# Kernel tuning notes

Hardware: AMD Instinct MI355X
Metric: run time of the kernel (lower is better)

Reference implementation:

```python
import jax, jax.numpy as jnp
import numpy as np
import math

N_CLASSES = 1000
CODE_LENGTH = 1024
IN_FEATURES = 4096
BATCH = 512
MAX_PROB = 0.95
POWER = 1.0


def _hadamard(n):
    # Sylvester construction; n must be a power of 2.
    H = np.array([[1.0]], dtype=np.float64)
    while H.shape[0] < n:
        H = np.block([[H, H], [H, -H]])
    return H


def setup_inputs() -> dict:
    key = jax.random.key(0)
    k1, k2, k3 = jax.random.split(key, 3)
    x = jax.random.normal(k1, (BATCH, IN_FEATURES), dtype=jnp.float32)
    out_feat = CODE_LENGTH - 1  # single head: code_length//1 - 1
    # nn.Linear default init: U(-1/sqrt(fan_in), 1/sqrt(fan_in))
    bound = 1.0 / math.sqrt(IN_FEATURES)
    W = jax.random.uniform(k2, (out_feat, IN_FEATURES), dtype=jnp.float32, minval=-bound, maxval=bound)
    b = jax.random.uniform(k3, (out_feat,), dtype=jnp.float32, minval=-bound, maxval=bound)
    labels = jnp.asarray(_hadamard(CODE_LENGTH)[:N_CLASSES, 1:], dtype=jnp.float32)  # (C, L-1)
    eps = jnp.float32(CODE_LENGTH * math.pow((1.0 - MAX_PROB) / (MAX_PROB * (N_CLASSES - 1)), 1.0 / POWER))
    power = jnp.float32(POWER)
    return {"x": x, "W": W, "b": b, "labels": labels, "eps": eps, "power": power}


def reference(x, W, b, labels, eps, power):
    # Linear head: (B, in) @ (in, L-1) + b
    h = jnp.tanh(x @ W.T + b)                               # (B, L-1)
    # L1 distance to each Hadamard code row: (B, 1, L-1) vs (C, L-1)
    d = jnp.sum(jnp.abs(h[:, None, :] - labels), axis=-1)   # (B, C)
    d = jnp.maximum(d, eps)
    inv = 1.0 / jnp.power(d, power)                          # (B, C)
    return inv / jnp.sum(inv, axis=-1, keepdims=True)
```

## Files before the change

### kernel.cpp

```cpp
#include <hip/hip_runtime.h>

#define BATCH 512
#define INFEAT 4096
#define LOUT 1023
#define NCLS 1000
#define NPAD 1024
#define SPLITK 8

typedef __bf16 bf16x8 __attribute__((ext_vector_type(8)));
typedef float f32x4 __attribute__((ext_vector_type(4)));

__device__ __forceinline__ unsigned short f2bf(float a) {
    unsigned u = __builtin_bit_cast(unsigned, a);
    return (unsigned short)((u + 0x7fffu + ((u >> 16) & 1u)) >> 16);
}
__device__ __forceinline__ unsigned f2bf2(float a, float b) {
    return (unsigned)f2bf(a) | ((unsigned)f2bf(b) << 16);
}
__device__ __forceinline__ float bf2f(unsigned short u) {
    return __builtin_bit_cast(float, ((unsigned)u) << 16);
}

__device__ __forceinline__ void gload_lds16(const void* g, void* l) {
    __builtin_amdgcn_global_load_lds(
        (const __attribute__((address_space(1))) void*)g,
        (__attribute__((address_space(3))) void*)l, 16, 0, 0);
}

__global__ __launch_bounds__(256) void k_cvt(const float* __restrict__ x,
                                             const float* __restrict__ W,
                                             unsigned char* __restrict__ xb,
                                             unsigned char* __restrict__ Wb) {
    int blk = blockIdx.x;
    if (blk < 1024) {
        int g = blk * 256 + threadIdx.x;
        int r = g >> 9, k16 = g & 511;
        const float4* p = (const float4*)(x + (size_t)r * INFEAT + k16 * 8);
        float4 v0 = p[0], v1 = p[1];
        uint4 o;
        o.x = f2bf2(v0.x, v0.y); o.y = f2bf2(v0.z, v0.w);
        o.z = f2bf2(v1.x, v1.y); o.w = f2bf2(v1.z, v1.w);
        *(uint4*)(xb + (size_t)r * 8192 + (k16 >> 3) * 128 + (((k16 & 7) ^ (r & 7)) * 16)) = o;
    } else {
        int g = (blk - 1024) * 256 + threadIdx.x;
        int r = g >> 9, k16 = g & 511;
        uint4 o = {0, 0, 0, 0};
        if (r < LOUT) {
            const float4* p = (const float4*)(W + (size_t)r * INFEAT + k16 * 8);
            float4 v0 = p[0], v1 = p[1];
            o.x = f2bf2(v0.x, v0.y); o.y = f2bf2(v0.z, v0.w);
            o.z = f2bf2(v1.x, v1.y); o.w = f2bf2(v1.z, v1.w);
        }
        *(uint4*)(Wb + (size_t)r * 8192 + (k16 >> 3) * 128 + (((k16 & 7) ^ (r & 7)) * 16)) = o;
    }
}

__global__ __launch_bounds__(256, 2) void k_gemm1(
    const unsigned char* __restrict__ xb, const unsigned char* __restrict__ Wb,
    unsigned short* __restrict__ partial) {
    __shared__ unsigned char lds[49152];
    f32x4 acc[4][2] = {};
    const int bn = blockIdx.x, bm = blockIdx.y, sp = blockIdx.z;
    const int tid = threadIdx.x;
    const int wave = tid >> 6, lane = tid & 63;
    const int lrow = lane & 15, lgrp = lane >> 4;
    const int wr = wave >> 1, wc = wave & 1;
    const int arow0 = bm * 128, brow0 = bn * 64, chunk0 = sp * 8;

    auto STAGE = [&](int bsel, int c) {
        unsigned char* lA = lds + bsel * 24576;
        unsigned char* lB = lA + 16384;
#pragma unroll
        for (int rr = 0; rr < 4; ++rr) {
            int g = rr * 256 + tid;
            int r = g >> 3, s = g & 7;
            gload_lds16(xb + (size_t)(arow0 + r) * 8192 + c * 128 + s * 16,
                        lA + (rr * 256 + wave * 64) * 16);
        }
#pragma unroll
        for (int rr = 0; rr < 2; ++rr) {
            int g = rr * 256 + tid;
            int r = g >> 3, s = g & 7;
            gload_lds16(Wb + (size_t)(brow0 + r) * 8192 + c * 128 + s * 16,
                        lB + (rr * 256 + wave * 64) * 16);
        }
    };

    auto COMPUTE = [&](int bsel) {
        const unsigned char* lA = lds + bsel * 24576;
        const unsigned char* lB = lA + 16384;
#pragma unroll
        for (int ks = 0; ks < 2; ++ks) {
            int swz = ((ks * 4 + lgrp) ^ (lrow & 7)) * 16;
            bf16x8 a[4], b[2];
#pragma unroll
            for (int m = 0; m < 4; ++m)
                a[m] = *(const bf16x8*)(lA + (wr * 64 + m * 16 + lrow) * 128 + swz);
#pragma unroll
            for (int n = 0; n < 2; ++n)
                b[n] = *(const bf16x8*)(lB + (wc * 32 + n * 16 + lrow) * 128 + swz);
#pragma unroll
            for (int m = 0; m < 4; ++m)
#pragma unroll
                for (int n = 0; n < 2; ++n)
                    acc[m][n] = __builtin_amdgcn_mfma_f32_16x16x32_bf16(
                        a[m], b[n], acc[m][n], 0, 0, 0);
        }
    };

    STAGE(0, chunk0);
    asm volatile("s_waitcnt vmcnt(0)" ::: "memory");
    __syncthreads();
#pragma unroll 1
    for (int t = 0; t < 8; ++t) {
        int cur = t & 1;
        if (t + 1 < 8) STAGE(cur ^ 1, chunk0 + t + 1);
        COMPUTE(cur);
        asm volatile("s_waitcnt vmcnt(0)" ::: "memory");
        __syncthreads();
    }

    unsigned short* P = partial + (size_t)sp * (BATCH * NPAD);
#pragma unroll
    for (int m = 0; m < 4; ++m)
#pragma unroll
        for (int n = 0; n < 2; ++n)
#pragma unroll
            for (int reg = 0; reg < 4; ++reg) {
                int r = arow0 + wr * 64 + m * 16 + lgrp * 4 + reg;
                int c = brow0 + wc * 32 + n * 16 + lrow;
                P[(size_t)r * NPAD + c] = f2bf(acc[m][n][reg]);
            }
}

__global__ __launch_bounds__(256) void k_fused(const unsigned short* __restrict__ partial,
                                               const float* __restrict__ bias,
                                               const float* __restrict__ epsp,
                                               const float* __restrict__ powp,
                                               float* __restrict__ out) {
    __shared__ float g[1024];
    __shared__ float wsum[4];
    const int r = blockIdx.x, t = threadIdx.x;
    const int n0 = t * 4;

    f32x4 v = {0.0f, 0.0f, 0.0f, 0.0f};
#pragma unroll
    for (int s = 0; s < SPLITK; ++s) {
        ushort4 p = *(const ushort4*)(partial + ((size_t)s * BATCH + r) * NPAD + n0);
        v[0] += bf2f(p.x); v[1] += bf2f(p.y); v[2] += bf2f(p.z); v[3] += bf2f(p.w);
    }
    float bb[4];
    if (t < 255) {
        float4 b4 = *(const float4*)(bias + n0);
        bb[0] = b4.x; bb[1] = b4.y; bb[2] = b4.z; bb[3] = b4.w;
    } else {
        bb[0] = bias[1020]; bb[1] = bias[1021]; bb[2] = bias[1022]; bb[3] = 0.0f;
    }
    if (t == 0) g[0] = 0.0f;
#pragma unroll
    for (int j = 0; j < 4; ++j) {
        int n = n0 + j;
        if (n < LOUT) g[n + 1] = tanhf(v[j] + bb[j]);
    }
    __syncthreads();

#pragma unroll 1
    for (int s = 0; s < 10; ++s) {
        int st = 1 << s;
#pragma unroll
        for (int pp = 0; pp < 2; ++pp) {
            int p = t + pp * 256;
            int idx = ((p >> s) << (s + 1)) | (p & (st - 1));
            float a = g[idx], c = g[idx + st];
            g[idx] = a + c;
            g[idx + st] = a - c;
        }
        __syncthreads();
    }

    const float eps = *epsp, pw = *powp;
    float iv[4];
    float ss = 0.0f;
#pragma unroll
    for (int j = 0; j < 4; ++j) {
        int c = n0 + j;
        float d = fmaxf(1023.0f - g[c], eps);
        float q = (pw == 1.0f) ? (1.0f / d) : powf(d, -pw);
        if (c >= NCLS) q = 0.0f;
        iv[j] = q;
        ss += q;
    }
#pragma unroll
    for (int m = 32; m; m >>= 1) ss += __shfl_xor(ss, m, 64);
    if ((t & 63) == 0) wsum[t >> 6] = ss;
    __syncthreads();
    float sc = 1.0f / (wsum[0] + wsum[1] + wsum[2] + wsum[3]);

    if (n0 < NCLS) {
        float4 o;
        o.x = iv[0] * sc; o.y = iv[1] * sc; o.z = iv[2] * sc; o.w = iv[3] * sc;
        *(float4*)(out + (size_t)r * NCLS + n0) = o;
    }
}

extern "C" void kernel_launch(void* const* d_in, const int* in_sizes, int n_in,
                              void* d_out, int out_size, void* d_ws, size_t ws_size,
                              hipStream_t stream) {
    const float* x = (const float*)d_in[0];
    const float* W = (const float*)d_in[1];
    const float* b = (const float*)d_in[2];
    const float* epsp = (const float*)d_in[4];
    const float* powp = (const float*)d_in[5];
    float* out = (float*)d_out;

    unsigned char* ws = (unsigned char*)d_ws;
    unsigned char* xb = ws;
    unsigned char* Wb = ws + (4u << 20);
    unsigned short* partial = (unsigned short*)(ws + (12u << 20));

    k_cvt<<<3072, 256, 0, stream>>>(x, W, xb, Wb);
    k_gemm1<<<dim3(16, 4, 8), 256, 0, stream>>>(xb, Wb, partial);
    k_fused<<<512, 256, 0, stream>>>(partial, b, epsp, powp, out);
}
```

Measured before the change: 27.93 us.

## Fuse split-K GEMM and epilogue via grid barrier, triple-buffer K stages

Merges the split-K GEMM and the tanh/Hadamard/normalize epilogue into one persistent 512-block kernel. A global atomic counter, reset by the conversion kernel, acts as a grid-wide barrier, so one launch is saved. The GEMM pipeline moves from double to triple buffering with partial vmcnt waits and raw barriers, keeping two loads in flight. Block indices are remapped so split-K slices interleave across CUs. This relies on all 512 blocks being co-resident: with 77.8KB LDS per block it could deadlock if occupancy is lower than assumed.

```diff
diff --git a/kernel.cpp b/kernel.cpp
--- a/kernel.cpp
+++ b/kernel.cpp
@@ -6,6 +6,7 @@
 #define NCLS 1000
 #define NPAD 1024
 #define SPLITK 8
+#define NBLK 512
 
 typedef __bf16 bf16x8 __attribute__((ext_vector_type(8)));
 typedef float f32x4 __attribute__((ext_vector_type(4)));
@@ -30,8 +31,10 @@
 __global__ __launch_bounds__(256) void k_cvt(const float* __restrict__ x,
                                              const float* __restrict__ W,
                                              unsigned char* __restrict__ xb,
-                                             unsigned char* __restrict__ Wb) {
+                                             unsigned char* __restrict__ Wb,
+                                             int* __restrict__ done) {
     int blk = blockIdx.x;
+    if (blk == 0 && threadIdx.x == 0) *done = 0;
     if (blk < 1024) {
         int g = blk * 256 + threadIdx.x;
         int r = g >> 9, k16 = g & 511;
@@ -55,32 +58,41 @@
     }
 }
 
-__global__ __launch_bounds__(256, 2) void k_gemm1(
+__global__ __launch_bounds__(256, 2) void k_gemm_fused(
     const unsigned char* __restrict__ xb, const unsigned char* __restrict__ Wb,
-    unsigned short* __restrict__ partial) {
-    __shared__ unsigned char lds[49152];
-    f32x4 acc[4][2] = {};
-    const int bn = blockIdx.x, bm = blockIdx.y, sp = blockIdx.z;
+    unsigned short* __restrict__ partial, const float* __restrict__ bias,
+    const float* __restrict__ epsp, const float* __restrict__ powp,
+    float* __restrict__ out, int* __restrict__ done) {
+    extern __shared__ __align__(16) unsigned char smem[];
+    unsigned char* lds = smem;
+    float* g = (float*)(smem + 73728);
+    float* wsum = (float*)(smem + 77824);
+
+    const int bid = blockIdx.x;
+    const int work = (bid & 7) * 64 + (bid >> 3);
+    const int bn = work & 15, bm = (work >> 4) & 3, sp = work >> 6;
     const int tid = threadIdx.x;
     const int wave = tid >> 6, lane = tid & 63;
     const int lrow = lane & 15, lgrp = lane >> 4;
     const int wr = wave >> 1, wc = wave & 1;
     const int arow0 = bm * 128, brow0 = bn * 64, chunk0 = sp * 8;
 
+    f32x4 acc[4][2] = {};
+
     auto STAGE = [&](int bsel, int c) {
         unsigned char* lA = lds + bsel * 24576;
         unsigned char* lB = lA + 16384;
 #pragma unroll
         for (int rr = 0; rr < 4; ++rr) {
-            int g = rr * 256 + tid;
-            int r = g >> 3, s = g & 7;
+            int gg = rr * 256 + tid;
+            int r = gg >> 3, s = gg & 7;
             gload_lds16(xb + (size_t)(arow0 + r) * 8192 + c * 128 + s * 16,
                         lA + (rr * 256 + wave * 64) * 16);
         }
 #pragma unroll
         for (int rr = 0; rr < 2; ++rr) {
-            int g = rr * 256 + tid;
-            int r = g >> 3, s = g & 7;
+            int gg = rr * 256 + tid;
+            int r = gg >> 3, s = gg & 7;
             gload_lds16(Wb + (size_t)(brow0 + r) * 8192 + c * 128 + s * 16,
                         lB + (rr * 256 + wave * 64) * 16);
         }
@@ -109,15 +121,23 @@
     };
 
     STAGE(0, chunk0);
-    asm volatile("s_waitcnt vmcnt(0)" ::: "memory");
-    __syncthreads();
+    STAGE(1, chunk0 + 1);
 #pragma unroll 1
     for (int t = 0; t < 8; ++t) {
-        int cur = t & 1;
-        if (t + 1 < 8) STAGE(cur ^ 1, chunk0 + t + 1);
-        COMPUTE(cur);
-        asm volatile("s_waitcnt vmcnt(0)" ::: "memory");
-        __syncthreads();
+        if (t < 6) {
+            STAGE((t + 2) % 3, chunk0 + t + 2);
+            asm volatile("s_waitcnt vmcnt(12)" ::: "memory");
+        } else if (t == 6) {
+            asm volatile("s_waitcnt vmcnt(6)" ::: "memory");
+        } else {
+            asm volatile("s_waitcnt vmcnt(0)" ::: "memory");
+        }
+        __builtin_amdgcn_s_barrier();
+        asm volatile("" ::: "memory");
+        COMPUTE(t % 3);
+        asm volatile("s_waitcnt lgkmcnt(0)" ::: "memory");
+        __builtin_amdgcn_s_barrier();
+        asm volatile("" ::: "memory");
     }
 
     unsigned short* P = partial + (size_t)sp * (BATCH * NPAD);
@@ -131,17 +151,20 @@
                 int c = brow0 + wc * 32 + n * 16 + lrow;
                 P[(size_t)r * NPAD + c] = f2bf(acc[m][n][reg]);
             }
-}
-
-__global__ __launch_bounds__(256) void k_fused(const unsigned short* __restrict__ partial,
-                                               const float* __restrict__ bias,
-                                               const float* __restrict__ epsp,
-                                               const float* __restrict__ powp,
-                                               float* __restrict__ out) {
-    __shared__ float g[1024];
-    __shared__ float wsum[4];
-    const int r = blockIdx.x, t = threadIdx.x;
-    const int n0 = t * 4;
+
+    __syncthreads();
+    if (tid == 0) {
+        __threadfence();
+        atomicAdd(done, 1);
+        while (__hip_atomic_load(done, __ATOMIC_RELAXED,
+                                 __HIP_MEMORY_SCOPE_AGENT) < NBLK)
+            __builtin_amdgcn_s_sleep(1);
+        __threadfence();
+    }
+    __syncthreads();
+
+    const int r = work;
+    const int n0 = tid * 4;
 
     f32x4 v = {0.0f, 0.0f, 0.0f, 0.0f};
 #pragma unroll
@@ -150,13 +173,13 @@
         v[0] += bf2f(p.x); v[1] += bf2f(p.y); v[2] += bf2f(p.z); v[3] += bf2f(p.w);
     }
     float bb[4];
-    if (t < 255) {
+    if (tid < 255) {
         float4 b4 = *(const float4*)(bias + n0);
         bb[0] = b4.x; bb[1] = b4.y; bb[2] = b4.z; bb[3] = b4.w;
     } else {
         bb[0] = bias[1020]; bb[1] = bias[1021]; bb[2] = bias[1022]; bb[3] = 0.0f;
     }
-    if (t == 0) g[0] = 0.0f;
+    if (tid == 0) g[0] = 0.0f;
 #pragma unroll
     for (int j = 0; j < 4; ++j) {
         int n = n0 + j;
@@ -169,7 +192,7 @@
         int st = 1 << s;
 #pragma unroll
         for (int pp = 0; pp < 2; ++pp) {
-            int p = t + pp * 256;
+            int p = tid + pp * 256;
             int idx = ((p >> s) << (s + 1)) | (p & (st - 1));
             float a = g[idx], c = g[idx + st];
             g[idx] = a + c;
@@ -192,7 +215,7 @@
     }
 #pragma unroll
     for (int m = 32; m; m >>= 1) ss += __shfl_xor(ss, m, 64);
-    if ((t & 63) == 0) wsum[t >> 6] = ss;
+    if ((tid & 63) == 0) wsum[tid >> 6] = ss;
     __syncthreads();
     float sc = 1.0f / (wsum[0] + wsum[1] + wsum[2] + wsum[3]);
 
@@ -217,8 +240,9 @@
     unsigned char* xb = ws;
     unsigned char* Wb = ws + (4u << 20);
     unsigned short* partial = (unsigned short*)(ws + (12u << 20));
-
-    k_cvt<<<3072, 256, 0, stream>>>(x, W, xb, Wb);
-    k_gemm1<<<dim3(16, 4, 8), 256, 0, stream>>>(xb, Wb, partial);
-    k_fused<<<512, 256, 0, stream>>>(partial, b, epsp, powp, out);
-}
+    int* done = (int*)(ws + (20u << 20));
+
+    k_cvt<<<3072, 256, 0, stream>>>(x, W, xb, Wb, done);
+    k_gemm_fused<<<NBLK, 256, 77840, stream>>>(xb, Wb, partial, b, epsp, powp,
+                                               out, done);
+}
```

Measured after the change: 62.95 us. 2.25x slower.

## Fuse fp32-to-bf16 conversion into GEMM loads via register staging

Applied to the files above, without the earlier changes.

Removes the separate conversion kernel. The GEMM now reads fp32 x and W directly into registers, packs them to bf16 and writes them into swizzled LDS, with the next chunk's global loads overlapping the current MFMA compute. It also remaps the block index so split-K slices are interleaved across the grid. This saves one launch and the bf16 workspace round trip. In exchange, each block reads twice the global bytes, uses more registers, and loses the asynchronous direct-to-LDS loads.

```diff
diff --git a/kernel.cpp b/kernel.cpp
--- a/kernel.cpp
+++ b/kernel.cpp
@@ -14,75 +14,77 @@
     unsigned u = __builtin_bit_cast(unsigned, a);
     return (unsigned short)((u + 0x7fffu + ((u >> 16) & 1u)) >> 16);
 }
-__device__ __forceinline__ unsigned f2bf2(float a, float b) {
-    return (unsigned)f2bf(a) | ((unsigned)f2bf(b) << 16);
-}
 __device__ __forceinline__ float bf2f(unsigned short u) {
     return __builtin_bit_cast(float, ((unsigned)u) << 16);
 }
 
-__device__ __forceinline__ void gload_lds16(const void* g, void* l) {
-    __builtin_amdgcn_global_load_lds(
-        (const __attribute__((address_space(1))) void*)g,
-        (__attribute__((address_space(3))) void*)l, 16, 0, 0);
-}
-
-__global__ __launch_bounds__(256) void k_cvt(const float* __restrict__ x,
-                                             const float* __restrict__ W,
-                                             unsigned char* __restrict__ xb,
-                                             unsigned char* __restrict__ Wb) {
-    int blk = blockIdx.x;
-    if (blk < 1024) {
-        int g = blk * 256 + threadIdx.x;
-        int r = g >> 9, k16 = g & 511;
-        const float4* p = (const float4*)(x + (size_t)r * INFEAT + k16 * 8);
-        float4 v0 = p[0], v1 = p[1];
-        uint4 o;
-        o.x = f2bf2(v0.x, v0.y); o.y = f2bf2(v0.z, v0.w);
-        o.z = f2bf2(v1.x, v1.y); o.w = f2bf2(v1.z, v1.w);
-        *(uint4*)(xb + (size_t)r * 8192 + (k16 >> 3) * 128 + (((k16 & 7) ^ (r & 7)) * 16)) = o;
-    } else {
-        int g = (blk - 1024) * 256 + threadIdx.x;
-        int r = g >> 9, k16 = g & 511;
-        uint4 o = {0, 0, 0, 0};
-        if (r < LOUT) {
-            const float4* p = (const float4*)(W + (size_t)r * INFEAT + k16 * 8);
-            float4 v0 = p[0], v1 = p[1];
-            o.x = f2bf2(v0.x, v0.y); o.y = f2bf2(v0.z, v0.w);
-            o.z = f2bf2(v1.x, v1.y); o.w = f2bf2(v1.z, v1.w);
-        }
-        *(uint4*)(Wb + (size_t)r * 8192 + (k16 >> 3) * 128 + (((k16 & 7) ^ (r & 7)) * 16)) = o;
-    }
-}
-
-__global__ __launch_bounds__(256, 2) void k_gemm1(
-    const unsigned char* __restrict__ xb, const unsigned char* __restrict__ Wb,
+__device__ __forceinline__ uint4 pack8(float4 a, float4 b) {
+    union { __bf16 h[8]; uint4 u; } r;
+    r.h[0] = (__bf16)a.x; r.h[1] = (__bf16)a.y;
+    r.h[2] = (__bf16)a.z; r.h[3] = (__bf16)a.w;
+    r.h[4] = (__bf16)b.x; r.h[5] = (__bf16)b.y;
+    r.h[6] = (__bf16)b.z; r.h[7] = (__bf16)b.w;
+    return r.u;
+}
+
+__global__ __launch_bounds__(256, 2) void k_gemm(
+    const float* __restrict__ x, const float* __restrict__ W,
     unsigned short* __restrict__ partial) {
     __shared__ unsigned char lds[49152];
-    f32x4 acc[4][2] = {};
-    const int bn = blockIdx.x, bm = blockIdx.y, sp = blockIdx.z;
+    const int bid = blockIdx.x;
+    const int work = (bid & 7) * 64 + (bid >> 3);
+    const int bn = work & 15, bm = (work >> 4) & 3, sp = work >> 6;
     const int tid = threadIdx.x;
     const int wave = tid >> 6, lane = tid & 63;
     const int lrow = lane & 15, lgrp = lane >> 4;
     const int wr = wave >> 1, wc = wave & 1;
     const int arow0 = bm * 128, brow0 = bn * 64, chunk0 = sp * 8;
 
-    auto STAGE = [&](int bsel, int c) {
+    f32x4 acc[4][2] = {};
+    float4 ar[4][2], br[2][2];
+
+    auto LOADR = [&](int t) {
+        const int c = chunk0 + t;
+#pragma unroll
+        for (int rr = 0; rr < 4; ++rr) {
+            int g = rr * 256 + tid;
+            int row = g >> 3, j = g & 7;
+            const float4* p = (const float4*)(x + (size_t)(arow0 + row) * INFEAT
+                                              + c * 64 + j * 8);
+            ar[rr][0] = p[0]; ar[rr][1] = p[1];
+        }
+#pragma unroll
+        for (int rr = 0; rr < 2; ++rr) {
+            int g = rr * 256 + tid;
+            int row = g >> 3, j = g & 7;
+            int wrow = brow0 + row;
+            if (wrow < LOUT) {
+                const float4* p = (const float4*)(W + (size_t)wrow * INFEAT
+                                                  + c * 64 + j * 8);
+                br[rr][0] = p[0]; br[rr][1] = p[1];
+            } else {
+                br[rr][0] = make_float4(0.f, 0.f, 0.f, 0.f);
+                br[rr][1] = make_float4(0.f, 0.f, 0.f, 0.f);
+            }
+        }
+    };
+
+    auto WRITE = [&](int bsel) {
         unsigned char* lA = lds + bsel * 24576;
         unsigned char* lB = lA + 16384;
 #pragma unroll
         for (int rr = 0; rr < 4; ++rr) {
             int g = rr * 256 + tid;
-            int r = g >> 3, s = g & 7;
-            gload_lds16(xb + (size_t)(arow0 + r) * 8192 + c * 128 + s * 16,
-                        lA + (rr * 256 + wave * 64) * 16);
+            int row = g >> 3, j = g & 7;
+            *(uint4*)(lA + row * 128 + ((j ^ (row & 7)) * 16)) =
+                pack8(ar[rr][0], ar[rr][1]);
         }
 #pragma unroll
         for (int rr = 0; rr < 2; ++rr) {
             int g = rr * 256 + tid;
-            int r = g >> 3, s = g & 7;
-            gload_lds16(Wb + (size_t)(brow0 + r) * 8192 + c * 128 + s * 16,
-                        lB + (rr * 256 + wave * 64) * 16);
+            int row = g >> 3, j = g & 7;
+            *(uint4*)(lB + row * 128 + ((j ^ (row & 7)) * 16)) =
+                pack8(br[rr][0], br[rr][1]);
         }
     };
 
@@ -108,15 +110,14 @@
         }
     };
 
-    STAGE(0, chunk0);
-    asm volatile("s_waitcnt vmcnt(0)" ::: "memory");
+    LOADR(0);
+    WRITE(0);
     __syncthreads();
 #pragma unroll 1
     for (int t = 0; t < 8; ++t) {
-        int cur = t & 1;
-        if (t + 1 < 8) STAGE(cur ^ 1, chunk0 + t + 1);
-        COMPUTE(cur);
-        asm volatile("s_waitcnt vmcnt(0)" ::: "memory");
+        if (t + 1 < 8) LOADR(t + 1);
+        COMPUTE(t & 1);
+        if (t + 1 < 8) WRITE((t + 1) & 1);
         __syncthreads();
     }
 
@@ -214,11 +215,8 @@
     float* out = (float*)d_out;
 
     unsigned char* ws = (unsigned char*)d_ws;
-    unsigned char* xb = ws;
-    unsigned char* Wb = ws + (4u << 20);
-    unsigned short* partial = (unsigned short*)(ws + (12u << 20));
-
-    k_cvt<<<3072, 256, 0, stream>>>(x, W, xb, Wb);
-    k_gemm1<<<dim3(16, 4, 8), 256, 0, stream>>>(xb, Wb, partial);
+    unsigned short* partial = (unsigned short*)ws;
+
+    k_gemm<<<512, 256, 0, stream>>>(x, W, partial);
     k_fused<<<512, 256, 0, stream>>>(partial, b, epsp, powp, out);
 }
```

Measured after the change: 26.83 us. -3.9%, faster.

## Shrink GEMM tile to 64x64, raise occupancy, remap block indices

Applied to the files above, without the earlier changes.

The split-K GEMM tile shrinks from 128x64 to 64x64, which doubles the grid to 1024 blocks. The shared-memory buffer and accumulators are reduced so more blocks fit per CU (launch bounds raised to 5). Blocks are remapped with an interleaved 1D index so that consecutive blocks are spread across split-K slices, and LDS fragment loads are hoisted ahead of the MFMA chain with setprio. The aim is better CU utilisation and latency hiding on a small GEMM, at the cost of more redundant global/LDS loads per FLOP.

```diff
diff --git a/kernel.cpp b/kernel.cpp
--- a/kernel.cpp
+++ b/kernel.cpp
@@ -55,79 +55,85 @@
     }
 }
 
-__global__ __launch_bounds__(256, 2) void k_gemm1(
+__global__ __launch_bounds__(256, 5) void k_gemm(
     const unsigned char* __restrict__ xb, const unsigned char* __restrict__ Wb,
     unsigned short* __restrict__ partial) {
-    __shared__ unsigned char lds[49152];
-    f32x4 acc[4][2] = {};
-    const int bn = blockIdx.x, bm = blockIdx.y, sp = blockIdx.z;
+    __shared__ unsigned char lds[32768];
+    const int bid = blockIdx.x;
+    const int work = (bid & 7) * 128 + (bid >> 3);
+    const int bn = work & 15, bm = (work >> 4) & 7, sp = work >> 7;
     const int tid = threadIdx.x;
     const int wave = tid >> 6, lane = tid & 63;
     const int lrow = lane & 15, lgrp = lane >> 4;
     const int wr = wave >> 1, wc = wave & 1;
-    const int arow0 = bm * 128, brow0 = bn * 64, chunk0 = sp * 8;
+    const int arow0 = bm * 64, brow0 = bn * 64, chunk0 = sp * 8;
+
+    const int g0 = wave * 2 * 64 + lane;
+    const int g1 = (wave * 2 + 1) * 64 + lane;
+    const int r0 = g0 >> 3, s0 = g0 & 7;
+    const int r1 = g1 >> 3, s1 = g1 & 7;
+
+    f32x4 acc[2][2] = {};
 
     auto STAGE = [&](int bsel, int c) {
-        unsigned char* lA = lds + bsel * 24576;
-        unsigned char* lB = lA + 16384;
-#pragma unroll
-        for (int rr = 0; rr < 4; ++rr) {
-            int g = rr * 256 + tid;
-            int r = g >> 3, s = g & 7;
-            gload_lds16(xb + (size_t)(arow0 + r) * 8192 + c * 128 + s * 16,
-                        lA + (rr * 256 + wave * 64) * 16);
-        }
-#pragma unroll
-        for (int rr = 0; rr < 2; ++rr) {
-            int g = rr * 256 + tid;
-            int r = g >> 3, s = g & 7;
-            gload_lds16(Wb + (size_t)(brow0 + r) * 8192 + c * 128 + s * 16,
-                        lB + (rr * 256 + wave * 64) * 16);
-        }
+        unsigned char* lA = lds + bsel * 16384;
+        unsigned char* lB = lA + 8192;
+        gload_lds16(xb + (size_t)(arow0 + r0) * 8192 + c * 128 + s0 * 16,
+                    lA + wave * 2048);
+        gload_lds16(xb + (size_t)(arow0 + r1) * 8192 + c * 128 + s1 * 16,
+                    lA + wave * 2048 + 1024);
+        gload_lds16(Wb + (size_t)(brow0 + r0) * 8192 + c * 128 + s0 * 16,
+                    lB + wave * 2048);
+        gload_lds16(Wb + (size_t)(brow0 + r1) * 8192 + c * 128 + s1 * 16,
+                    lB + wave * 2048 + 1024);
     };
 
     auto COMPUTE = [&](int bsel) {
-        const unsigned char* lA = lds + bsel * 24576;
-        const unsigned char* lB = lA + 16384;
+        const unsigned char* lA = lds + bsel * 16384;
+        const unsigned char* lB = lA + 8192;
+        bf16x8 fa[2][2], fb[2][2];
 #pragma unroll
         for (int ks = 0; ks < 2; ++ks) {
             int swz = ((ks * 4 + lgrp) ^ (lrow & 7)) * 16;
-            bf16x8 a[4], b[2];
-#pragma unroll
-            for (int m = 0; m < 4; ++m)
-                a[m] = *(const bf16x8*)(lA + (wr * 64 + m * 16 + lrow) * 128 + swz);
+#pragma unroll
+            for (int m = 0; m < 2; ++m)
+                fa[ks][m] = *(const bf16x8*)(lA + (wr * 32 + m * 16 + lrow) * 128 + swz);
 #pragma unroll
             for (int n = 0; n < 2; ++n)
-                b[n] = *(const bf16x8*)(lB + (wc * 32 + n * 16 + lrow) * 128 + swz);
-#pragma unroll
-            for (int m = 0; m < 4; ++m)
+                fb[ks][n] = *(const bf16x8*)(lB + (wc * 32 + n * 16 + lrow) * 128 + swz);
+        }
+        __builtin_amdgcn_s_setprio(1);
+#pragma unroll
+        for (int ks = 0; ks < 2; ++ks)
+#pragma unroll
+            for (int m = 0; m < 2; ++m)
 #pragma unroll
                 for (int n = 0; n < 2; ++n)
                     acc[m][n] = __builtin_amdgcn_mfma_f32_16x16x32_bf16(
-                        a[m], b[n], acc[m][n], 0, 0, 0);
-        }
+                        fa[ks][m], fb[ks][n], acc[m][n], 0, 0, 0);
+        __builtin_amdgcn_s_setprio(0);
     };
 
     STAGE(0, chunk0);
     asm volatile("s_waitcnt vmcnt(0)" ::: "memory");
-    __syncthreads();
+    __builtin_amdgcn_s_barrier();
 #pragma unroll 1
     for (int t = 0; t < 8; ++t) {
-        int cur = t & 1;
+        const int cur = t & 1;
         if (t + 1 < 8) STAGE(cur ^ 1, chunk0 + t + 1);
         COMPUTE(cur);
-        asm volatile("s_waitcnt vmcnt(0)" ::: "memory");
-        __syncthreads();
+        asm volatile("s_waitcnt vmcnt(0) lgkmcnt(0)" ::: "memory");
+        __builtin_amdgcn_s_barrier();
     }
 
     unsigned short* P = partial + (size_t)sp * (BATCH * NPAD);
 #pragma unroll
-    for (int m = 0; m < 4; ++m)
+    for (int m = 0; m < 2; ++m)
 #pragma unroll
         for (int n = 0; n < 2; ++n)
 #pragma unroll
             for (int reg = 0; reg < 4; ++reg) {
-                int r = arow0 + wr * 64 + m * 16 + lgrp * 4 + reg;
+                int r = arow0 + wr * 32 + m * 16 + lgrp * 4 + reg;
                 int c = brow0 + wc * 32 + n * 16 + lrow;
                 P[(size_t)r * NPAD + c] = f2bf(acc[m][n][reg]);
             }
@@ -219,6 +225,6 @@
     unsigned short* partial = (unsigned short*)(ws + (12u << 20));
 
     k_cvt<<<3072, 256, 0, stream>>>(x, W, xb, Wb);
-    k_gemm1<<<dim3(16, 4, 8), 256, 0, stream>>>(xb, Wb, partial);
+    k_gemm<<<1024, 256, 0, stream>>>(xb, Wb, partial);
     k_fused<<<512, 256, 0, stream>>>(partial, b, epsp, powp, out);
 }
```

New measurement: 27.38 us. No clear change (-2.0%).
